# Performance work log

Measured on AMD Instinct MI355X. Metric: run time of the kernel, lower is better.

Reference implementation:

```python
import jax, jax.numpy as jnp
import numpy as np

SEQ, B, V, E, H, L = 64, 64, 32000, 512, 512, 2


def setup_inputs() -> dict:
    key = jax.random.key(0)
    ks = jax.random.split(key, 12)
    k = float(np.sqrt(1.0 / H))
    u = lambda kk, shape, a, b: jax.random.uniform(kk, shape, jnp.float32, a, b)
    return {
        "inputs": jax.random.randint(ks[0], (SEQ, B), 0, V),          # [T, B] token ids
        "hidden": jnp.zeros((L, B, H), jnp.float32),                   # initial hidden
        "emb": u(ks[1], (V, E), -0.1, 0.1),                            # embedding table
        "Wr_w": u(ks[2], (L, H, E + H), -k, k),                        # reset gate [L,H,2H]
        "Wr_b": u(ks[3], (L, H), -k, k),
        "Wz_w": u(ks[4], (L, H, E + H), -k, k),                        # update gate
        "Wz_b": u(ks[5], (L, H), -k, k),
        "Wh_w": u(ks[6], (L, H, E + H), -k, k),                        # candidate
        "Wh_b": u(ks[7], (L, H), -k, k),
        "out_w": u(ks[8], (V, H), -0.1, 0.1),                          # output projection
        "out_b": jnp.zeros((V,), jnp.float32),
    }


def reference(inputs, hidden, emb, Wr_w, Wr_b, Wz_w, Wz_b, Wh_w, Wh_b, out_w, out_b):
    # GRU recurrence over time via lax.scan (dropout disabled: dp_keep_prob=1.0)
    def step(h, tok):
        x = emb[tok]  # [B, E]
        new_h = []
        for i in range(L):  # fixed small layer loop
            hi = h[i]  # [B, H]
            cat = jnp.concatenate([x, hi], axis=1)  # [B, E+H]
            r = jax.nn.sigmoid(cat @ Wr_w[i].T + Wr_b[i])
            z = jax.nn.sigmoid(cat @ Wz_w[i].T + Wz_b[i])
            h_hat = jnp.tanh(jnp.concatenate([x, r * hi], axis=1) @ Wh_w[i].T + Wh_b[i])
            x = (1.0 - z) * hi + z * h_hat  # next layer input / new hidden
            new_h.append(x)
        logits_t = x @ out_w.T + out_b  # [B, V]
        return jnp.stack(new_h), logits_t

    hidden_final, logits = jax.lax.scan(step, hidden, inputs)
    return logits, hidden_final  # [T,B,V], [L,B,H]
```

## Files before the change

### kernel.cpp

```cpp
#include <hip/hip_runtime.h>

constexpr int NT = 64;
constexpr int NB = 64;
constexpr int NV = 32000;
constexpr int NE = 512;
constexpr int NH = 512;
constexpr int NQUAD = 16 * 125;

constexpr size_t SZ_OW  = (size_t)NV * NE;
constexpr size_t SZ_XE  = (size_t)NT * NB * NE;
constexpr size_t SZ_H   = (size_t)NB * NH;
constexpr size_t LOGITS = (size_t)NT * NB * NV;

typedef float f32x4 __attribute__((ext_vector_type(4)));
typedef int   i32x4 __attribute__((ext_vector_type(4)));
typedef short bf16x8 __attribute__((ext_vector_type(8)));
typedef short s16x4 __attribute__((ext_vector_type(4)));
typedef _Float16 f16x8 __attribute__((ext_vector_type(8)));

__device__ __forceinline__ unsigned short f2bf(float x) {
  unsigned u = __float_as_uint(x);
  u += 0x7FFFu + ((u >> 16) & 1u);
  return (unsigned short)(u >> 16);
}
__device__ __forceinline__ float bf2f(unsigned short s) {
  return __uint_as_float(((unsigned)s) << 16);
}
__device__ __forceinline__ void split2(float v, short* hi, short* lo) {
  unsigned short h = f2bf(v);
  *hi = (short)h;
  *lo = (short)f2bf(v - bf2f(h));
}
__device__ __forceinline__ f32x4 mma_bf16(bf16x8 a, bf16x8 b, f32x4 c) {
  return __builtin_amdgcn_mfma_f32_16x16x32_bf16(a, b, c, 0, 0, 0);
}
__device__ __forceinline__ f32x4 mma_f16(f16x8 a, f16x8 b, f32x4 c) {
  return __builtin_amdgcn_mfma_f32_16x16x32_f16(a, b, c, 0, 0, 0);
}
__device__ __forceinline__ float fast_sigmoid(float x) {
  return __builtin_amdgcn_rcpf(1.0f + __expf(-x));
}
__device__ __forceinline__ float fast_tanh(float x) {
  return 1.0f - 2.0f * __builtin_amdgcn_rcpf(1.0f + __expf(2.0f * x));
}

__device__ __forceinline__ void st_sc32u(unsigned* p, unsigned v) {
  asm volatile("global_store_dword %0, %1, off sc0 sc1" :: "v"(p), "v"(v) : "memory");
}
__device__ __forceinline__ void st_sc128(void* p, i32x4 v) {
  asm volatile("global_store_dwordx4 %0, %1, off sc0 sc1" :: "v"(p), "v"(v) : "memory");
}
__device__ __forceinline__ void st_nt(float* p, float v) {
  asm volatile("global_store_dword %0, %1, off nt" :: "v"(p), "v"(v) : "memory");
}
__device__ __forceinline__ unsigned ld_sc32u(const unsigned* p) {
  unsigned v;
  asm volatile("global_load_dword %0, %1, off sc0 sc1\n\ts_waitcnt vmcnt(0)"
               : "=v"(v) : "v"(p) : "memory");
  return v;
}

__device__ __forceinline__ void wave_poll(const unsigned* fp, unsigned thr) {
  while (!__all((int)(ld_sc32u(fp) >= thr))) {}
}
__device__ __forceinline__ void wave_poll4(const unsigned* flags, int slotBase, int cgBase,
                                           int rh, unsigned thr, int lane) {
  const unsigned* fp = &flags[(size_t)(slotBase + (cgBase + (lane & 3)) * 2 + rh) * 32];
  wave_poll(fp, thr);
}

__device__ __forceinline__ void publish(unsigned* flags, int slot, unsigned val) {
  asm volatile("s_waitcnt vmcnt(0)" ::: "memory");
  __syncthreads();
  if (threadIdx.x == 0) st_sc32u(&flags[(size_t)slot * 32], val);
}

__global__ void k_prep(
    const float* __restrict__ outw, const int* __restrict__ toks,
    const float* __restrict__ emb, const float* __restrict__ hid,
    _Float16* OWf, short* XeHi, short* XeLo,
    short* X1Hi, short* X1Lo, short* h0Hi, short* h0Lo) {
  const size_t stride = (size_t)gridDim.x * blockDim.x;
  const size_t N1 = SZ_OW, N2 = N1 + SZ_XE, N3 = N2 + SZ_H, N4 = N3 + SZ_H;
  for (size_t x = (size_t)blockIdx.x * blockDim.x + threadIdx.x; x < N4; x += stride) {
    if (x < N1) {
      OWf[x] = (_Float16)outw[x];
    } else if (x < N2) {
      size_t p = x - N1;
      size_t r = p >> 9, c = p & 511u;
      int tok = toks[r];
      float v = emb[(size_t)tok * 512 + c];
      short hi, lo; split2(v, &hi, &lo);
      XeHi[p] = hi; XeLo[p] = lo;
    } else if (x < N3) {
      size_t p = x - N2;
      short hi, lo; split2(hid[p], &hi, &lo);
      h0Hi[p] = hi; h0Lo[p] = lo;
    } else {
      size_t p = x - N3;
      short hi, lo; split2(hid[SZ_H + p], &hi, &lo);
      X1Hi[p] = hi; X1Lo[p] = lo;
    }
  }
}

__device__ __forceinline__ void mmaP32(
    const short* __restrict__ aH, const short* __restrict__ aL, int base,
    const short* lsHi_, const short* lsLo_,
    f32x4 (&accH)[2], f32x4 (&accL)[2], int wave, int l15, int lq) {
  const int kq = wave >> 1, rhalf = wave & 1;
  const int r0 = rhalf * 16 + l15;
#pragma unroll
  for (int i = 0; i < 4; ++i) {
    const int ko = kq * 128 + i * 32 + lq * 8;
    const int kg = base + ko;
    const int e0 = (l15 * 1024 + kg) ^ ((l15 & 7) << 3);
    const int e1 = ((16 + l15) * 1024 + kg) ^ ((l15 & 7) << 3);
    bf16x8 bh0 = *(const bf16x8*)&lsHi_[e0];
    bf16x8 bl0 = *(const bf16x8*)&lsLo_[e0];
    bf16x8 bh1 = *(const bf16x8*)&lsHi_[e1];
    bf16x8 bl1 = *(const bf16x8*)&lsLo_[e1];
    bf16x8 ah = *(const bf16x8*)&aH[r0 * 512 + ko];
    bf16x8 al = *(const bf16x8*)&aL[r0 * 512 + ko];
    accH[0] = mma_bf16(ah, bh0, accH[0]);
    accH[1] = mma_bf16(ah, bh1, accH[1]);
    accL[0] = mma_bf16(al, bh0, accL[0]);
    accL[1] = mma_bf16(al, bh1, accL[1]);
    accL[0] = mma_bf16(ah, bl0, accL[0]);
    accL[1] = mma_bf16(ah, bl1, accL[1]);
  }
}
__device__ __forceinline__ void reduce4(float* lsRed_, f32x4 (&accH)[2], f32x4 (&accL)[2],
                                        f32x4 (&acc)[2], int wave, int l15, int lq) {
  const int kq = wave >> 1, rhalf = wave & 1;
  acc[0] = accH[0] + accL[0];
  acc[1] = accH[1] + accL[1];
  const int pos = l15 * 16 + lq * 4;
  if (kq) {
    *(f32x4*)&lsRed_[(((kq - 1) * 2 + rhalf) * 2 + 0) * 256 + pos] = acc[0];
    *(f32x4*)&lsRed_[(((kq - 1) * 2 + rhalf) * 2 + 1) * 256 + pos] = acc[1];
  }
  __syncthreads();
  if (!kq) {
#pragma unroll
    for (int s = 0; s < 3; ++s) {
      acc[0] += *(const f32x4*)&lsRed_[((s * 2 + rhalf) * 2 + 0) * 256 + pos];
      acc[1] += *(const f32x4*)&lsRed_[((s * 2 + rhalf) * 2 + 1) * 256 + pos];
    }
  }
  __syncthreads();
}

__device__ __forceinline__ void mmaD(
    const short* __restrict__ pAH, const short* __restrict__ pAL,
    int kloc0, int kkGlob0, const short* lsHi_, const short* lsLo_,
    f32x4 (&accH)[2], f32x4 (&accL)[2], int l15, int lq, int rhalf, int rowbase) {
  const int r0 = rowbase + rhalf * 16 + l15;
#pragma unroll 4
  for (int i = 0; i < 8; ++i) {
    const int kk = kkGlob0 + i * 32 + lq * 8;
    const int ka = kloc0 + i * 32 + lq * 8;
    const int e0 = (l15 * 1024 + kk) ^ ((l15 & 7) << 3);
    const int e1 = ((16 + l15) * 1024 + kk) ^ ((l15 & 7) << 3);
    bf16x8 bh0 = *(const bf16x8*)&lsHi_[e0];
    bf16x8 bl0 = *(const bf16x8*)&lsLo_[e0];
    bf16x8 bh1 = *(const bf16x8*)&lsHi_[e1];
    bf16x8 bl1 = *(const bf16x8*)&lsLo_[e1];
    bf16x8 ah = *(const bf16x8*)&pAH[r0 * 512 + ka];
    bf16x8 al = *(const bf16x8*)&pAL[r0 * 512 + ka];
    accH[0] = mma_bf16(ah, bh0, accH[0]);
    accH[1] = mma_bf16(ah, bh1, accH[1]);
    accL[0] = mma_bf16(al, bh0, accL[0]);
    accL[1] = mma_bf16(al, bh1, accL[1]);
    accL[0] = mma_bf16(ah, bl0, accL[0]);
    accL[1] = mma_bf16(ah, bl1, accL[1]);
  }
}
__device__ __forceinline__ void reduceD(float* lsRed_, f32x4 (&accH)[2], f32x4 (&accL)[2],
                                        f32x4 (&acc)[2], int wave, int l15, int lq) {
  acc[0] = accH[0] + accL[0];
  acc[1] = accH[1] + accL[1];
  const int pos = l15 * 16 + lq * 4;
  if (wave >= 2) {
    *(f32x4*)&lsRed_[((wave - 2) * 2 + 0) * 256 + pos] = acc[0];
    *(f32x4*)&lsRed_[((wave - 2) * 2 + 1) * 256 + pos] = acc[1];
  }
  __syncthreads();
  if (wave < 2) {
#pragma unroll
    for (int s = 0; s < 3; ++s) {
      const int slot = (wave & 1) + 2 * s;
      acc[0] += *(const f32x4*)&lsRed_[(slot * 2 + 0) * 256 + pos];
      acc[1] += *(const f32x4*)&lsRed_[(slot * 2 + 1) * 256 + pos];
    }
  }
  __syncthreads();
}

__device__ __forceinline__ void stage_weights(
    short* lsHi, short* lsLo, const float* srcBase0, const float* srcBase1,
    int jc, int tid) {
  for (int i = tid; i < 8192; i += 512) {
    const int j = i >> 8;
    const int k4 = (i & 255) << 2;
    const int g = jc + j;
    const float* src = (srcBase1 && g >= 512)
        ? (srcBase1 + (size_t)(g - 512) * 1024 + k4)
        : (srcBase0 + (size_t)g * 1024 + k4);
    f32x4 v = *(const f32x4*)src;
    s16x4 h4, l4;
#pragma unroll
    for (int q = 0; q < 4; ++q) { short hi, lo; split2(v[q], &hi, &lo); h4[q] = hi; l4[q] = lo; }
    const int els = (j * 1024 + k4) ^ ((j & 7) << 3);
    *(s16x4*)&lsHi[els] = h4;
    *(s16x4*)&lsLo[els] = l4;
  }
}

__device__ void gemm_loop(char* pool, int tid,
                          const _Float16* Af, const _Float16* Bw,
                          const float* bias, float* C,
                          unsigned* flags, unsigned* tcnt) {
  _Float16* lsA0 = (_Float16*)pool;
  _Float16* lsA1 = lsA0 + 8192;
  _Float16* lsB0 = lsA1 + 8192;
  _Float16* lsB1 = lsB0 + 8192;
  volatile int* bc = (volatile int*)(pool + 65536);
  const int wave = tid >> 6, lane = tid & 63, l15 = lane & 15, lq = lane >> 4;
  const int wr = (wave >> 2) * 64, wc = (wave & 3) * 32;
  unsigned lastR = 0;
  __syncthreads();
  for (;;) {
    if (tid == 0)
      *bc = (int)__hip_atomic_fetch_add(tcnt, 1u, __ATOMIC_RELAXED,
                                        __HIP_MEMORY_SCOPE_AGENT);
    __syncthreads();
    const int pr = *bc;
    __syncthreads();
    if (pr >= NQUAD) break;
    const int p = pr / 125, bq = pr - p * 125;
    const unsigned Rneed = 4u * (unsigned)p + 4u;
    if (lastR < Rneed) {
      if (tid < 32) {
        const unsigned* fp = &flags[(size_t)(160 + tid) * 32];
        while (ld_sc32u(fp) < Rneed) __builtin_amdgcn_s_sleep(8);
      }
      lastR = Rneed;
    }
    __syncthreads();
    f32x4 a00[4][2] = {}, a01[4][2] = {}, a10[4][2] = {}, a11[4][2] = {};
    const size_t arow0 = (size_t)p * 256;
    const size_t brow0 = (size_t)bq * 256;
    for (int kb = 0; kb < 512; kb += 64) {
#pragma unroll
      for (int i = 0; i < 2; ++i) {
        int c = tid + i * 512;
        int row = c >> 3, kc = (c & 7) * 8;
        int el = (row * 64 + kc) ^ ((row & 7) << 3);
        *(f16x8*)&lsA0[el] = *(const f16x8*)(Af + (arow0 + row) * 512 + kb + kc);
        *(f16x8*)&lsA1[el] = *(const f16x8*)(Af + (arow0 + 128 + row) * 512 + kb + kc);
        *(f16x8*)&lsB0[el] = *(const f16x8*)(Bw + (brow0 + row) * 512 + kb + kc);
        *(f16x8*)&lsB1[el] = *(const f16x8*)(Bw + (brow0 + 128 + row) * 512 + kb + kc);
      }
      __syncthreads();
#pragma unroll
      for (int k0 = 0; k0 < 64; k0 += 32) {
        const int kk = k0 + lq * 8;
        f16x8 af0[4], af1[4], b0[2], b1[2];
#pragma unroll
        for (int i = 0; i < 4; ++i) {
          int ra = wr + i * 16 + l15;
          int el = (ra * 64 + kk) ^ ((ra & 7) << 3);
          af0[i] = *(const f16x8*)&lsA0[el];
          af1[i] = *(const f16x8*)&lsA1[el];
        }
#pragma unroll
        for (int jt = 0; jt < 2; ++jt) {
          int rb = wc + jt * 16 + l15;
          int el = (rb * 64 + kk) ^ ((rb & 7) << 3);
          b0[jt] = *(const f16x8*)&lsB0[el];
          b1[jt] = *(const f16x8*)&lsB1[el];
        }
#pragma unroll
        for (int i = 0; i < 4; ++i)
#pragma unroll
          for (int jt = 0; jt < 2; ++jt) {
            a00[i][jt] = mma_f16(af0[i], b0[jt], a00[i][jt]);
            a01[i][jt] = mma_f16(af0[i], b1[jt], a01[i][jt]);
            a10[i][jt] = mma_f16(af1[i], b0[jt], a10[i][jt]);
            a11[i][jt] = mma_f16(af1[i], b1[jt], a11[i][jt]);
          }
      }
      __syncthreads();
    }
    const float c00 = bias[brow0 + wc + l15];
    const float c01 = bias[brow0 + wc + 16 + l15];
    const float c10 = bias[brow0 + 128 + wc + l15];
    const float c11 = bias[brow0 + 128 + wc + 16 + l15];
#pragma unroll
    for (int i = 0; i < 4; ++i) {
#pragma unroll
      for (int r = 0; r < 4; ++r) {
        const size_t row = arow0 + wr + i * 16 + lq * 4 + r;
        float* pa = C + row * (size_t)NV + brow0 + wc + l15;
        st_nt(pa, a00[i][0][r] + c00);
        st_nt(pa + 16, a00[i][1][r] + c01);
        st_nt(pa + 128, a01[i][0][r] + c10);
        st_nt(pa + 144, a01[i][1][r] + c11);
        float* pb = pa + (size_t)128 * NV;
        st_nt(pb, a10[i][0][r] + c00);
        st_nt(pb + 16, a10[i][1][r] + c01);
        st_nt(pb + 128, a11[i][0][r] + c10);
        st_nt(pb + 144, a11[i][1][r] + c11);
      }
    }
  }
}

__launch_bounds__(512, 1)
__global__ void k_main(
    const float* __restrict__ Wr, const float* __restrict__ Wz, const float* __restrict__ Wh,
    const float* __restrict__ Wrb, const float* __restrict__ Wzb, const float* __restrict__ Whb,
    const short* __restrict__ XeHi, const short* __restrict__ XeLo,
    short* X1Hi, short* X1Lo, _Float16* X1f16,
    short* h0Hi, short* h0Lo,
    short* rh0Hi, short* rh0Lo, short* rh1Hi, short* rh1Lo,
    float* z0, float* z1, float* hidOut,
    const _Float16* OWf, const float* outb, float* out,
    unsigned* flags, unsigned* tcnt) {
  __shared__ __align__(16) char pool[153600];
  short* lsHi = (short*)pool;
  short* lsLo = lsHi + 32 * 1024;
  float* lsRed = (float*)(pool + 131072);
  short* sH    = (short*)(pool + 131072);
  short* sL    = sH + 1024;
  float* sZA   = (float*)(pool + 131072);
  short* stH   = (short*)(pool + 143360);
  short* stL   = stH + 1024;
  float* sZ    = (float*)(pool + 147456);
  _Float16* sX = (_Float16*)(pool + 151552);

  const int wg = blockIdx.x;
  const int tid = threadIdx.x;
  const int wave = tid >> 6, lane = tid & 63, l15 = lane & 15, lq = lane >> 4;

  if (wg < 64) {
    const int cg = wg >> 1, rh = wg & 1, jc = cg * 32, rowbase = rh * 32;
    const bool isR = (jc < 512);
    stage_weights(lsHi, lsLo, Wr, Wz, jc, tid);
    float biasL0, biasL1;
    {
      const int j0 = jc + l15, j1 = j0 + 16;
      biasL0 = (j0 < 512) ? Wrb[j0] : Wzb[j0 - 512];
      biasL1 = (j1 < 512) ? Wrb[j1] : Wzb[j1 - 512];
    }
    __syncthreads();
    for (int t = 0; t < NT; ++t) {
      f32x4 accH[2] = {}, accL[2] = {};
      mmaP32(XeHi + (size_t)t * SZ_H + rowbase * 512,
             XeLo + (size_t)t * SZ_H + rowbase * 512, 0,
             lsHi, lsLo, accH, accL, wave, l15, lq);
      const short* hH = h0Hi + (size_t)t * SZ_H + rowbase * 512;
      const short* hL = h0Lo + (size_t)t * SZ_H + rowbase * 512;
      {
        const int idx = lane & 7;
        int cgp = 4 * (wave >> 1) + (idx & 3);
        if (idx == 4 && isR) cgp = (jc >> 5);
        const unsigned* fp = &flags[(size_t)(128 + cgp * 2 + rh) * 32];
        wave_poll(fp, (unsigned)t);
      }
      i32x4 pre;
      const int pbuf = tid >> 7, pq = tid & 127, prow = pq >> 2, pc = pq & 3;
      if (isR && tid < 256)
        pre = *(const i32x4*)((pbuf ? hL : hH) + prow * 512 + jc + pc * 8);
      mmaP32(hH, hL, 512, lsHi, lsLo, accH, accL, wave, l15, lq);
      if (isR && tid < 256)
        *(i32x4*)&(pbuf ? stL : stH)[prow * 32 + pc * 8] = pre;
      f32x4 acc[2];
      reduce4(lsRed, accH, accL, acc, wave, l15, lq);
      if (wave < 2) {
#pragma unroll
        for (int ct = 0; ct < 2; ++ct) {
          const int jj = ct * 16 + l15;
          const float bv = ct ? biasL1 : biasL0;
#pragma unroll
          for (int r = 0; r < 4; ++r) {
            const int lb = wave * 16 + lq * 4 + r;
            const float s = fast_sigmoid(acc[ct][r] + bv);
            if (isR) {
              const float hv = bf2f((unsigned short)stH[lb * 32 + jj]) +
                               bf2f((unsigned short)stL[lb * 32 + jj]);
              short hi, lo; split2(s * hv, &hi, &lo);
              sH[lb * 32 + jj] = hi; sL[lb * 32 + jj] = lo;
            } else {
              sZA[lb * 32 + jj] = s;
            }
          }
        }
      }
      __syncthreads();
      if (isR) {
        if (tid < 256) {
          i32x4 v = *(const i32x4*)&(pbuf ? sL : sH)[prow * 32 + pc * 8];
          st_sc128((pbuf ? rh0Lo : rh0Hi) + (size_t)t * SZ_H +
                   (size_t)(rowbase + prow) * 512 + jc + pc * 8, v);
        }
      } else {
        if (tid < 256) {
          const int row = tid >> 3, c = tid & 7;
          i32x4 v = *(const i32x4*)&sZA[row * 32 + c * 4];
          st_sc128(z0 + (size_t)t * SZ_H + (size_t)(rowbase + row) * 512 +
                   (jc - 512) + c * 4, v);
        }
      }
      publish(flags, wg, (unsigned)(t + 1));
    }
  } else if (wg < 128) {
    const int idx0 = wg - 64, cg = idx0 >> 1, rh = idx0 & 1, jc = cg * 32, rowbase = (idx0 & 1) * 32;
    const bool isR = (jc < 512);
    stage_weights(lsHi, lsLo, Wr + (size_t)512 * 1024, Wz + (size_t)512 * 1024, jc, tid);
    float biasL0, biasL1;
    {
      const int j0 = jc + l15, j1 = j0 + 16;
      biasL0 = (j0 < 512) ? Wrb[512 + j0] : Wzb[512 + j0 - 512];
      biasL1 = (j1 < 512) ? Wrb[512 + j1] : Wzb[512 + j1 - 512];
    }
    __syncthreads();
    for (int t = 0; t < NT; ++t) {
      const short* xH = h0Hi + (size_t)(t + 1) * SZ_H;
      const short* xL = h0Lo + (size_t)(t + 1) * SZ_H;
      const short* hH = X1Hi + (size_t)t * SZ_H;
      const short* hL = X1Lo + (size_t)t * SZ_H;
      const int khalf = wave >> 1, rhalf = wave & 1;
      {
        const int idx = lane & 15;
        const unsigned* fp; unsigned thr;
        if (idx == 8 && isR) {
          fp = &flags[(size_t)(160 + (jc >> 5) * 2 + rh) * 32]; thr = (unsigned)t;
        } else if (khalf < 2) {
          const int cgp = (khalf & 1) * 8 + (idx & 7);
          fp = &flags[(size_t)(128 + cgp * 2 + rh) * 32]; thr = (unsigned)(t + 1);
        } else {
          const int cgp = (khalf & 1) * 8 + (idx & 7);
          fp = &flags[(size_t)(160 + cgp * 2 + rh) * 32]; thr = (unsigned)t;
        }
        wave_poll(fp, thr);
      }
      i32x4 pre;
      const int pbuf = tid >> 7, pq = tid & 127, prow = pq >> 2, pc = pq & 3;
      if (isR && tid < 256)
        pre = *(const i32x4*)((pbuf ? hL : hH) +
                              (size_t)(rowbase + prow) * 512 + jc + pc * 8);
      f32x4 accH[2] = {}, accL[2] = {};
      {
        const short* pAH = (khalf < 2) ? xH : hH;
        const short* pAL = (khalf < 2) ? xL : hL;
        mmaD(pAH, pAL, (khalf & 1) * 256, khalf * 256, lsHi, lsLo,
             accH, accL, l15, lq, rhalf, rowbase);
      }
      if (isR && tid < 256)
        *(i32x4*)&(pbuf ? stL : stH)[prow * 32 + pc * 8] = pre;
      f32x4 acc[2];
      reduceD(lsRed, accH, accL, acc, wave, l15, lq);
      if (wave < 2) {
#pragma unroll
        for (int ct = 0; ct < 2; ++ct) {
          const int jj = ct * 16 + l15;
          const float bv = ct ? biasL1 : biasL0;
#pragma unroll
          for (int r = 0; r < 4; ++r) {
            const int lb = wave * 16 + lq * 4 + r;
            const float s = fast_sigmoid(acc[ct][r] + bv);
            if (isR) {
              const float hv = bf2f((unsigned short)stH[lb * 32 + jj]) +
                               bf2f((unsigned short)stL[lb * 32 + jj]);
              short hi, lo; split2(s * hv, &hi, &lo);
              sH[lb * 32 + jj] = hi; sL[lb * 32 + jj] = lo;
            } else {
              sZA[lb * 32 + jj] = s;
            }
          }
        }
      }
      __syncthreads();
      if (isR) {
        if (tid < 256) {
          i32x4 v = *(const i32x4*)&(pbuf ? sL : sH)[prow * 32 + pc * 8];
          st_sc128((pbuf ? rh1Lo : rh1Hi) + (size_t)t * SZ_H +
                   (size_t)(rowbase + prow) * 512 + jc + pc * 8, v);
        }
      } else {
        if (tid < 256) {
          const int row = tid >> 3, c = tid & 7;
          i32x4 v = *(const i32x4*)&sZA[row * 32 + c * 4];
          st_sc128(z1 + (size_t)t * SZ_H + (size_t)(rowbase + row) * 512 +
                   (jc - 512) + c * 4, v);
        }
      }
      publish(flags, wg, (unsigned)(t + 1));
    }
  } else if (wg < 192) {
    const bool isL1 = (wg >= 160);
    const int idx0 = isL1 ? (wg - 160) : (wg - 128);
    const int cg = idx0 >> 1, rh = idx0 & 1, jc = cg * 32, rowbase = (idx0 & 1) * 32;
    const int layer = isL1 ? 1 : 0;
    stage_weights(lsHi, lsLo, Wh + (size_t)layer * 512 * 1024, nullptr, jc, tid);
    const float biasL0 = Whb[layer * 512 + jc + l15];
    const float biasL1 = Whb[layer * 512 + jc + 16 + l15];
    __syncthreads();
    short* myHi = isL1 ? X1Hi : h0Hi;
    short* myLo = isL1 ? X1Lo : h0Lo;
    const short* rhHi_ = isL1 ? rh1Hi : rh0Hi;
    const short* rhLo_ = isL1 ? rh1Lo : rh0Lo;
    const float* zArr = isL1 ? z1 : z0;
    const int fbase = isL1 ? 64 : 0;
    for (int t = 0; t < NT; ++t) {
      const int pbuf = tid >> 7, pq = tid & 127, prow = pq >> 2, pc = pq & 3;
      if (tid < 256) {
        const short* src = (pbuf ? myLo : myHi) + (size_t)t * SZ_H +
                           (size_t)(rowbase + prow) * 512 + jc + pc * 8;
        *(i32x4*)&(pbuf ? stL : stH)[prow * 32 + pc * 8] = *(const i32x4*)src;
      }
      f32x4 accH[2] = {}, accL[2] = {};
      if (isL1) {
        wave_poll4(flags, 128, 4 * (wave >> 1), rh, (unsigned)(t + 1), lane);
        mmaP32(h0Hi + (size_t)(t + 1) * SZ_H + rowbase * 512,
               h0Lo + (size_t)(t + 1) * SZ_H + rowbase * 512, 0,
               lsHi, lsLo, accH, accL, wave, l15, lq);
      } else {
        mmaP32(XeHi + (size_t)t * SZ_H + rowbase * 512,
               XeLo + (size_t)t * SZ_H + rowbase * 512, 0,
               lsHi, lsLo, accH, accL, wave, l15, lq);
      }
      {
        const int idx = lane & 7;
        int cgp = 4 * (wave >> 1) + (idx & 3);
        if (idx == 4) cgp = 16 + (jc >> 5);
        const unsigned* fp = &flags[(size_t)(fbase + cgp * 2 + rh) * 32];
        wave_poll(fp, (unsigned)(t + 1));
      }
      f32x4 zv;
      const int zrow = tid >> 3, zc = tid & 7;
      if (tid < 256)
        zv = *(const f32x4*)(zArr + (size_t)t * SZ_H +
                             (size_t)(rowbase + zrow) * 512 + jc + zc * 4);
      mmaP32(rhHi_ + (size_t)t * SZ_H + rowbase * 512,
             rhLo_ + (size_t)t * SZ_H + rowbase * 512, 512,
             lsHi, lsLo, accH, accL, wave, l15, lq);
      if (tid < 256)
        *(f32x4*)&sZ[zrow * 32 + zc * 4] = zv;
      f32x4 acc[2];
      reduce4(lsRed, accH, accL, acc, wave, l15, lq);
      if (wave < 2) {
#pragma unroll
        for (int ct = 0; ct < 2; ++ct) {
          const int jj = ct * 16 + l15, j = jc + jj;
          const float bv = ct ? biasL1 : biasL0;
#pragma unroll
          for (int r = 0; r < 4; ++r) {
            const int lb = wave * 16 + lq * 4 + r;
            const float hh = fast_tanh(acc[ct][r] + bv);
            const float z = sZ[lb * 32 + jj];
            const float ho = bf2f((unsigned short)stH[lb * 32 + jj]) +
                             bf2f((unsigned short)stL[lb * 32 + jj]);
            const float hn = (1.0f - z) * ho + z * hh;
            short hi, lo; split2(hn, &hi, &lo);
            sH[lb * 32 + jj] = hi; sL[lb * 32 + jj] = lo;
            if (isL1) sX[lb * 32 + jj] = (_Float16)hn;
            if (t == NT - 1)
              hidOut[(size_t)layer * SZ_H + (size_t)(rowbase + lb) * 512 + j] = hn;
          }
        }
      }
      __syncthreads();
      if (tid < 256) {
        i32x4 v = *(const i32x4*)&(pbuf ? sL : sH)[prow * 32 + pc * 8];
        st_sc128((pbuf ? myLo : myHi) + (size_t)(t + 1) * SZ_H +
                 (size_t)(rowbase + prow) * 512 + jc + pc * 8, v);
      } else if (isL1 && tid < 384) {
        const int q = tid - 256, row = q >> 2, c = q & 3;
        i32x4 v = *(const i32x4*)&sX[row * 32 + c * 8];
        st_sc128(X1f16 + (size_t)t * SZ_H + (size_t)(rowbase + row) * 512 + jc + c * 8, v);
      }
      publish(flags, wg, (unsigned)(t + 1));
    }
  }
  gemm_loop(pool, tid, X1f16, OWf, outb, out, flags, tcnt);
}

extern "C" void kernel_launch(void* const* d_in, const int* in_sizes, int n_in,
                              void* d_out, int out_size, void* d_ws, size_t ws_size,
                              hipStream_t stream) {
  (void)in_sizes; (void)n_in; (void)out_size; (void)ws_size;
  const int*   toks = (const int*)d_in[0];
  const float* hid  = (const float*)d_in[1];
  const float* emb  = (const float*)d_in[2];
  const float* Wr   = (const float*)d_in[3];
  const float* Wrb  = (const float*)d_in[4];
  const float* Wz   = (const float*)d_in[5];
  const float* Wzb  = (const float*)d_in[6];
  const float* Wh   = (const float*)d_in[7];
  const float* Whb  = (const float*)d_in[8];
  const float* outw = (const float*)d_in[9];
  const float* outb = (const float*)d_in[10];
  float* out = (float*)d_out;

  char* base = (char*)d_ws;
  size_t off = 0;
  auto carve = [&](size_t bytes) -> char* {
    char* r = base + off;
    off = (off + bytes + 255) & ~(size_t)255;
    return r;
  };
  _Float16* OWf   = (_Float16*)carve(SZ_OW * 2);
  short*    XeHi  = (short*)carve(SZ_XE * 2);
  short*    XeLo  = (short*)carve(SZ_XE * 2);
  short*    X1Hi  = (short*)carve((size_t)(NT + 1) * SZ_H * 2);
  short*    X1Lo  = (short*)carve((size_t)(NT + 1) * SZ_H * 2);
  _Float16* X1f16 = (_Float16*)carve((size_t)NT * SZ_H * 2);
  short*    h0Hi  = (short*)carve((size_t)(NT + 1) * SZ_H * 2);
  short*    h0Lo  = (short*)carve((size_t)(NT + 1) * SZ_H * 2);
  short*    rh0Hi = (short*)carve((size_t)NT * SZ_H * 2);
  short*    rh0Lo = (short*)carve((size_t)NT * SZ_H * 2);
  short*    rh1Hi = (short*)carve((size_t)NT * SZ_H * 2);
  short*    rh1Lo = (short*)carve((size_t)NT * SZ_H * 2);
  float*    z0    = (float*)carve((size_t)NT * SZ_H * 4);
  float*    z1    = (float*)carve((size_t)NT * SZ_H * 4);
  unsigned* flags = (unsigned*)carve(32768);
  unsigned* tcnt  = (unsigned*)carve(256);

  hipMemsetAsync(flags, 0, 32768, stream);
  hipMemsetAsync(tcnt, 0, 256, stream);

  k_prep<<<2048, 256, 0, stream>>>(outw, toks, emb, hid,
                                   OWf, XeHi, XeLo, X1Hi, X1Lo, h0Hi, h0Lo);

  k_main<<<256, 512, 0, stream>>>(
      Wr, Wz, Wh, Wrb, Wzb, Whb, XeHi, XeLo,
      X1Hi, X1Lo, X1f16, h0Hi, h0Lo,
      rh0Hi, rh0Lo, rh1Hi, rh1Lo, z0, z1,
      out + LOGITS, OWf, outb, out, flags, tcnt);
}
```

Measured before the change: 703.2 us.

## Halve output-GEMM B tile to 128 columns and hoist A-fragment loads in recurrence MMAs

The output-projection GEMM tile shrinks from 256x256 to 256x128, doubling the number of dynamically scheduled work items (4000 instead of 2000) and cutting LDS and accumulator use per tile. The aim is finer-grained load balancing and overlap with the recurrence, at the cost of reloading the A tile twice as often. Separately, the recurrent MMA helpers (mmaP32, mmaD) load all A fragments from global memory in a batch before the MFMA loop, so that load latency can overlap. This raises register pressure in those helpers.

```diff
diff --git a/kernel.cpp b/kernel.cpp
--- a/kernel.cpp
+++ b/kernel.cpp
@@ -5,7 +5,7 @@
 constexpr int NV = 32000;
 constexpr int NE = 512;
 constexpr int NH = 512;
-constexpr int NQUAD = 16 * 125;
+constexpr int NPAIR = 16 * 250;
 
 constexpr size_t SZ_OW  = (size_t)NV * NE;
 constexpr size_t SZ_XE  = (size_t)NT * NB * NE;
@@ -110,24 +110,28 @@
     f32x4 (&accH)[2], f32x4 (&accL)[2], int wave, int l15, int lq) {
   const int kq = wave >> 1, rhalf = wave & 1;
   const int r0 = rhalf * 16 + l15;
+  bf16x8 ah[4], al[4];
 #pragma unroll
   for (int i = 0; i < 4; ++i) {
     const int ko = kq * 128 + i * 32 + lq * 8;
-    const int kg = base + ko;
+    ah[i] = *(const bf16x8*)&aH[r0 * 512 + ko];
+    al[i] = *(const bf16x8*)&aL[r0 * 512 + ko];
+  }
+#pragma unroll
+  for (int i = 0; i < 4; ++i) {
+    const int kg = base + kq * 128 + i * 32 + lq * 8;
     const int e0 = (l15 * 1024 + kg) ^ ((l15 & 7) << 3);
     const int e1 = ((16 + l15) * 1024 + kg) ^ ((l15 & 7) << 3);
     bf16x8 bh0 = *(const bf16x8*)&lsHi_[e0];
     bf16x8 bl0 = *(const bf16x8*)&lsLo_[e0];
     bf16x8 bh1 = *(const bf16x8*)&lsHi_[e1];
     bf16x8 bl1 = *(const bf16x8*)&lsLo_[e1];
-    bf16x8 ah = *(const bf16x8*)&aH[r0 * 512 + ko];
-    bf16x8 al = *(const bf16x8*)&aL[r0 * 512 + ko];
-    accH[0] = mma_bf16(ah, bh0, accH[0]);
-    accH[1] = mma_bf16(ah, bh1, accH[1]);
-    accL[0] = mma_bf16(al, bh0, accL[0]);
-    accL[1] = mma_bf16(al, bh1, accL[1]);
-    accL[0] = mma_bf16(ah, bl0, accL[0]);
-    accL[1] = mma_bf16(ah, bl1, accL[1]);
+    accH[0] = mma_bf16(ah[i], bh0, accH[0]);
+    accH[1] = mma_bf16(ah[i], bh1, accH[1]);
+    accL[0] = mma_bf16(al[i], bh0, accL[0]);
+    accL[1] = mma_bf16(al[i], bh1, accL[1]);
+    accL[0] = mma_bf16(ah[i], bl0, accL[0]);
+    accL[1] = mma_bf16(ah[i], bl1, accL[1]);
   }
 }
 __device__ __forceinline__ void reduce4(float* lsRed_, f32x4 (&accH)[2], f32x4 (&accL)[2],
@@ -156,24 +160,31 @@
     int kloc0, int kkGlob0, const short* lsHi_, const short* lsLo_,
     f32x4 (&accH)[2], f32x4 (&accL)[2], int l15, int lq, int rhalf, int rowbase) {
   const int r0 = rowbase + rhalf * 16 + l15;
-#pragma unroll 4
-  for (int i = 0; i < 8; ++i) {
-    const int kk = kkGlob0 + i * 32 + lq * 8;
-    const int ka = kloc0 + i * 32 + lq * 8;
-    const int e0 = (l15 * 1024 + kk) ^ ((l15 & 7) << 3);
-    const int e1 = ((16 + l15) * 1024 + kk) ^ ((l15 & 7) << 3);
-    bf16x8 bh0 = *(const bf16x8*)&lsHi_[e0];
-    bf16x8 bl0 = *(const bf16x8*)&lsLo_[e0];
-    bf16x8 bh1 = *(const bf16x8*)&lsHi_[e1];
-    bf16x8 bl1 = *(const bf16x8*)&lsLo_[e1];
-    bf16x8 ah = *(const bf16x8*)&pAH[r0 * 512 + ka];
-    bf16x8 al = *(const bf16x8*)&pAL[r0 * 512 + ka];
-    accH[0] = mma_bf16(ah, bh0, accH[0]);
-    accH[1] = mma_bf16(ah, bh1, accH[1]);
-    accL[0] = mma_bf16(al, bh0, accL[0]);
-    accL[1] = mma_bf16(al, bh1, accL[1]);
-    accL[0] = mma_bf16(ah, bl0, accL[0]);
-    accL[1] = mma_bf16(ah, bl1, accL[1]);
+#pragma unroll
+  for (int b = 0; b < 2; ++b) {
+    bf16x8 ah[4], al[4];
+#pragma unroll
+    for (int i = 0; i < 4; ++i) {
+      const int ka = kloc0 + (b * 4 + i) * 32 + lq * 8;
+      ah[i] = *(const bf16x8*)&pAH[r0 * 512 + ka];
+      al[i] = *(const bf16x8*)&pAL[r0 * 512 + ka];
+    }
+#pragma unroll
+    for (int i = 0; i < 4; ++i) {
+      const int kk = kkGlob0 + (b * 4 + i) * 32 + lq * 8;
+      const int e0 = (l15 * 1024 + kk) ^ ((l15 & 7) << 3);
+      const int e1 = ((16 + l15) * 1024 + kk) ^ ((l15 & 7) << 3);
+      bf16x8 bh0 = *(const bf16x8*)&lsHi_[e0];
+      bf16x8 bl0 = *(const bf16x8*)&lsLo_[e0];
+      bf16x8 bh1 = *(const bf16x8*)&lsHi_[e1];
+      bf16x8 bl1 = *(const bf16x8*)&lsLo_[e1];
+      accH[0] = mma_bf16(ah[i], bh0, accH[0]);
+      accH[1] = mma_bf16(ah[i], bh1, accH[1]);
+      accL[0] = mma_bf16(al[i], bh0, accL[0]);
+      accL[1] = mma_bf16(al[i], bh1, accL[1]);
+      accL[0] = mma_bf16(ah[i], bl0, accL[0]);
+      accL[1] = mma_bf16(ah[i], bl1, accL[1]);
+    }
   }
 }
 __device__ __forceinline__ void reduceD(float* lsRed_, f32x4 (&accH)[2], f32x4 (&accL)[2],
@@ -222,10 +233,9 @@
                           const float* bias, float* C,
                           unsigned* flags, unsigned* tcnt) {
   _Float16* lsA0 = (_Float16*)pool;
-  _Float16* lsA1 = lsA0 + 8192;
-  _Float16* lsB0 = lsA1 + 8192;
-  _Float16* lsB1 = lsB0 + 8192;
-  volatile int* bc = (volatile int*)(pool + 65536);
+  _Float16* lsA1 = lsA0 + 128 * 64;
+  _Float16* lsB  = lsA1 + 128 * 64;
+  volatile int* bc = (volatile int*)(pool + 49152);
   const int wave = tid >> 6, lane = tid & 63, l15 = lane & 15, lq = lane >> 4;
   const int wr = (wave >> 2) * 64, wc = (wave & 3) * 32;
   unsigned lastR = 0;
@@ -237,8 +247,8 @@
     __syncthreads();
     const int pr = *bc;
     __syncthreads();
-    if (pr >= NQUAD) break;
-    const int p = pr / 125, bq = pr - p * 125;
+    if (pr >= NPAIR) break;
+    const int p = pr / 250, bn = pr - p * 250;
     const unsigned Rneed = 4u * (unsigned)p + 4u;
     if (lastR < Rneed) {
       if (tid < 32) {
@@ -248,9 +258,9 @@
       lastR = Rneed;
     }
     __syncthreads();
-    f32x4 a00[4][2] = {}, a01[4][2] = {}, a10[4][2] = {}, a11[4][2] = {};
+    f32x4 acc0[4][2] = {}, acc1[4][2] = {};
     const size_t arow0 = (size_t)p * 256;
-    const size_t brow0 = (size_t)bq * 256;
+    const size_t brow0 = (size_t)bn * 128;
     for (int kb = 0; kb < 512; kb += 64) {
 #pragma unroll
       for (int i = 0; i < 2; ++i) {
@@ -259,14 +269,13 @@
         int el = (row * 64 + kc) ^ ((row & 7) << 3);
         *(f16x8*)&lsA0[el] = *(const f16x8*)(Af + (arow0 + row) * 512 + kb + kc);
         *(f16x8*)&lsA1[el] = *(const f16x8*)(Af + (arow0 + 128 + row) * 512 + kb + kc);
-        *(f16x8*)&lsB0[el] = *(const f16x8*)(Bw + (brow0 + row) * 512 + kb + kc);
-        *(f16x8*)&lsB1[el] = *(const f16x8*)(Bw + (brow0 + 128 + row) * 512 + kb + kc);
+        *(f16x8*)&lsB[el]  = *(const f16x8*)(Bw + (brow0 + row) * 512 + kb + kc);
       }
       __syncthreads();
 #pragma unroll
       for (int k0 = 0; k0 < 64; k0 += 32) {
         const int kk = k0 + lq * 8;
-        f16x8 af0[4], af1[4], b0[2], b1[2];
+        f16x8 af0[4], af1[4], bfr[2];
 #pragma unroll
         for (int i = 0; i < 4; ++i) {
           int ra = wr + i * 16 + l15;
@@ -277,41 +286,31 @@
 #pragma unroll
         for (int jt = 0; jt < 2; ++jt) {
           int rb = wc + jt * 16 + l15;
-          int el = (rb * 64 + kk) ^ ((rb & 7) << 3);
-          b0[jt] = *(const f16x8*)&lsB0[el];
-          b1[jt] = *(const f16x8*)&lsB1[el];
+          bfr[jt] = *(const f16x8*)&lsB[(rb * 64 + kk) ^ ((rb & 7) << 3)];
         }
 #pragma unroll
         for (int i = 0; i < 4; ++i)
 #pragma unroll
           for (int jt = 0; jt < 2; ++jt) {
-            a00[i][jt] = mma_f16(af0[i], b0[jt], a00[i][jt]);
-            a01[i][jt] = mma_f16(af0[i], b1[jt], a01[i][jt]);
-            a10[i][jt] = mma_f16(af1[i], b0[jt], a10[i][jt]);
-            a11[i][jt] = mma_f16(af1[i], b1[jt], a11[i][jt]);
+            acc0[i][jt] = mma_f16(af0[i], bfr[jt], acc0[i][jt]);
+            acc1[i][jt] = mma_f16(af1[i], bfr[jt], acc1[i][jt]);
           }
       }
       __syncthreads();
     }
-    const float c00 = bias[brow0 + wc + l15];
-    const float c01 = bias[brow0 + wc + 16 + l15];
-    const float c10 = bias[brow0 + 128 + wc + l15];
-    const float c11 = bias[brow0 + 128 + wc + 16 + l15];
+    const float b0v = bias[brow0 + wc + l15];
+    const float b1v = bias[brow0 + wc + 16 + l15];
 #pragma unroll
     for (int i = 0; i < 4; ++i) {
 #pragma unroll
       for (int r = 0; r < 4; ++r) {
         const size_t row = arow0 + wr + i * 16 + lq * 4 + r;
         float* pa = C + row * (size_t)NV + brow0 + wc + l15;
-        st_nt(pa, a00[i][0][r] + c00);
-        st_nt(pa + 16, a00[i][1][r] + c01);
-        st_nt(pa + 128, a01[i][0][r] + c10);
-        st_nt(pa + 144, a01[i][1][r] + c11);
+        st_nt(pa, acc0[i][0][r] + b0v);
+        st_nt(pa + 16, acc0[i][1][r] + b1v);
         float* pb = pa + (size_t)128 * NV;
-        st_nt(pb, a10[i][0][r] + c00);
-        st_nt(pb + 16, a10[i][1][r] + c01);
-        st_nt(pb + 128, a11[i][0][r] + c10);
-        st_nt(pb + 144, a11[i][1][r] + c11);
+        st_nt(pb, acc1[i][0][r] + b0v);
+        st_nt(pb + 16, acc1[i][1][r] + b1v);
       }
     }
   }
```

Measured after the change: 697.0 us. Within noise of the previous version (-0.9%).
